# Kernel optimization log

Hardware: AMD Instinct MI355X
Metric: run time of the kernel (lower is better)

Reference implementation:

```python
import jax, jax.numpy as jnp
import numpy as np

TILE = 128
NEG = -1e10


def rotate_half(x):
    half = x.shape[-1] // 2
    return jnp.concatenate([-x[..., half:], x[..., :half]], axis=-1)


def setup_inputs() -> dict:
    key = jax.random.key(0)
    ks = jax.random.split(key, 7)
    B, S, E, H, D, K = 1, 4096, 2048, 16, 128, 8
    T = S // TILE
    x = jax.random.normal(ks[0], (B, S, E), jnp.float32)
    wq = jax.random.normal(ks[1], (E, H * D), jnp.float32) * 0.02
    wk = jax.random.normal(ks[2], (E, H * D), jnp.float32) * 0.02
    wv = jax.random.normal(ks[3], (E, H * D), jnp.float32) * 0.02
    wo = jax.random.normal(ks[4], (H * D, E), jnp.float32) * 0.02
    rope_angles = jax.random.uniform(ks[5], (S, D // 2), jnp.float32)
    anchor_indices = jax.random.randint(ks[6], (B, H, T, K), 0, T).astype(jnp.int32)
    return {"x": x, "wq": wq, "wk": wk, "wv": wv, "wo": wo,
            "rope_angles": rope_angles, "anchor_indices": anchor_indices}


def reference(x, wq, wk, wv, wo, rope_angles, anchor_indices):
    B, S, E = x.shape
    D = rope_angles.shape[1] * 2          # head_dim
    H = wq.shape[1] // D                  # num_heads
    T = S // TILE                         # num_tiles
    sm_scale = 1.0 / jnp.sqrt(jnp.float32(D))

    # QKV projections -> [B, H, S, D]
    def proj(w):
        return (x @ w).reshape(B, S, H, D).transpose(0, 2, 1, 3).astype(jnp.float32)
    q, k, v = proj(wq), proj(wk), proj(wv)

    # RoPE (half-split / rotate_half format)
    cos = jnp.cos(rope_angles)[None, None]   # [1,1,S,D/2]
    sin = jnp.sin(rope_angles)[None, None]
    cos_f = jnp.concatenate([cos, cos], axis=-1)
    sin_f = jnp.concatenate([sin, sin], axis=-1)
    q = q * cos_f + rotate_half(q) * sin_f
    k = k * cos_f + rotate_half(k) * sin_f

    # Tile selection: anchor tiles + local (diagonal) tile -> [B,H,T,K+1]
    local = jnp.broadcast_to(jnp.arange(T, dtype=jnp.int32)[None, None, :, None], (B, H, T, 1))
    tile_sel = jnp.concatenate([anchor_indices, local], axis=-1)
    L = tile_sel.shape[-1] * TILE            # sparse_len
    token_idx = tile_sel[..., None] * TILE + jnp.arange(TILE, dtype=jnp.int32)[None, None, None, None, :]
    flat_idx = jnp.clip(token_idx.reshape(B, H, T, L), 0, S - 1)  # [B,H,T,L]

    # Gather selected KV tiles: [B,H,T,L,D]
    def gather(kv):
        return jnp.take_along_axis(kv, flat_idx.reshape(B, H, T * L, 1), axis=2).reshape(B, H, T, L, D)
    k_sp, v_sp = gather(k), gather(v)

    # Block-sparse attention per query tile
    q_t = q.reshape(B, H, T, TILE, D)
    logits = jnp.einsum('bhtqd,bhtkd->bhtqk', q_t, k_sp) * sm_scale
    q_pos = jnp.arange(S).reshape(T, TILE)
    future = flat_idx[:, :, :, None, :] > q_pos[None, None, :, :, None]  # causal mask on gathered keys
    logits = jnp.where(future, NEG, logits)
    w = jax.nn.softmax(logits, axis=-1)
    all_masked = jnp.all(future, axis=-1, keepdims=True)
    w = jnp.where(all_masked, 0.0, w)
    w = jnp.where(jnp.isnan(w), 0.0, w)
    out = jnp.einsum('bhtqk,bhtkd->bhtqd', w, v_sp)

    out = out.reshape(B, H, S, D).transpose(0, 2, 1, 3).reshape(B, S, H * D)
    return out @ wo
```

## Files before the change

kernel.cpp:

```cpp
#include <hip/hip_runtime.h>
#include <stdint.h>

typedef unsigned short u16;
typedef unsigned int u32;

#define S_LEN 4096
#define EMB 2048
#define NH 16
#define HD 128
#define HDTOT 2048
#define T_TILES 32
#define KANCH 8
#define SM_SCALE 0.088388347648318447f

typedef __bf16 bf16x8 __attribute__((ext_vector_type(8)));
typedef float f32x4 __attribute__((ext_vector_type(4)));

typedef const __attribute__((address_space(1))) u32 ga_u32;
typedef __attribute__((address_space(3))) u32 lds_u32;

__device__ __forceinline__ u16 f2bf(float f) {
  u32 b = __builtin_bit_cast(u32, f);
  b = (b + 0x7FFFu + ((b >> 16) & 1u)) >> 16;
  return (u16)b;
}
__device__ __forceinline__ float bf2f(u16 u) {
  return __builtin_bit_cast(float, ((u32)u) << 16);
}
__device__ __forceinline__ f32x4 mfma16(bf16x8 a, bf16x8 b, f32x4 c) {
  return __builtin_amdgcn_mfma_f32_16x16x32_bf16(a, b, c, 0, 0, 0);
}

#define ASM_LGKM0 do { asm volatile("s_waitcnt lgkmcnt(0)" ::: "memory"); \
                       __builtin_amdgcn_sched_barrier(0); } while (0)
#define ASM_VMC(n) do { asm volatile("s_waitcnt vmcnt(" #n ")" ::: "memory"); \
                        __builtin_amdgcn_sched_barrier(0); } while (0)

__global__ __launch_bounds__(256) void k_prep(
    const float* __restrict__ x, u16* __restrict__ xb,
    const float* __restrict__ w0, const float* __restrict__ w1,
    const float* __restrict__ w2, const float* __restrict__ w3,
    u16* __restrict__ o0, u16* __restrict__ o1,
    u16* __restrict__ o2, u16* __restrict__ o3,
    const float* __restrict__ ang, float2* __restrict__ tab) {
  __shared__ float tile[64][68];
  const int bid = blockIdx.x;
  const int tid = threadIdx.x;
  if (bid < 8192) {
    int i = (bid * 256 + tid) * 4;
    float4 v = *(const float4*)(x + i);
    ushort4 o;
    o.x = f2bf(v.x); o.y = f2bf(v.y); o.z = f2bf(v.z); o.w = f2bf(v.w);
    *(ushort4*)(xb + i) = o;
  } else if (bid < 12288) {
    int idx = bid - 8192;
    int z = idx >> 10, rem = idx & 1023;
    int n0 = (rem & 31) * 64, k0 = (rem >> 5) * 64;
    const float* w; u16* o;
    if (z == 0)      { w = w0; o = o0; }
    else if (z == 1) { w = w1; o = o1; }
    else if (z == 2) { w = w2; o = o2; }
    else             { w = w3; o = o3; }
    int r = tid >> 4, cq = (tid & 15) << 2;
    for (int p = 0; p < 4; ++p) {
      float4 v = *(const float4*)(w + (size_t)(k0 + r + p * 16) * EMB + n0 + cq);
      tile[r + p * 16][cq + 0] = v.x;
      tile[r + p * 16][cq + 1] = v.y;
      tile[r + p * 16][cq + 2] = v.z;
      tile[r + p * 16][cq + 3] = v.w;
    }
    __syncthreads();
    for (int p = 0; p < 4; ++p) {
      int rn = r + p * 16;
      ushort4 u;
      u.x = f2bf(tile[cq + 0][rn]);
      u.y = f2bf(tile[cq + 1][rn]);
      u.z = f2bf(tile[cq + 2][rn]);
      u.w = f2bf(tile[cq + 3][rn]);
      *(ushort4*)(o + (size_t)(n0 + rn) * EMB + k0 + cq) = u;
    }
  } else {
    int i = (bid - 12288) * 256 + tid;
    float a = ang[i];
    float s, c;
    __sincosf(a, &s, &c);
    tab[i] = make_float2(c, s);
  }
}

__global__ __launch_bounds__(256) void k_transpose_v(const u16* __restrict__ v,
                                                     u16* __restrict__ vt) {
  __shared__ u16 tile[64][72];
  int n0 = blockIdx.x * 64, s0 = blockIdx.y * 64;
  int tid = threadIdx.x;
  int r = tid >> 4, cq = (tid & 15) << 2;
  for (int p = 0; p < 4; ++p) {
    ushort4 u = *(const ushort4*)(v + (size_t)(s0 + r + p * 16) * HDTOT + n0 + cq);
    tile[r + p * 16][cq + 0] = u.x;
    tile[r + p * 16][cq + 1] = u.y;
    tile[r + p * 16][cq + 2] = u.z;
    tile[r + p * 16][cq + 3] = u.w;
  }
  __syncthreads();
  for (int p = 0; p < 4; ++p) {
    int rn = r + p * 16;
    ushort4 o;
    o.x = tile[cq + 0][rn];
    o.y = tile[cq + 1][rn];
    o.z = tile[cq + 2][rn];
    o.w = tile[cq + 3][rn];
    *(ushort4*)(vt + (size_t)(n0 + rn) * S_LEN + s0 + cq) = o;
  }
}

template <bool BF16OUT>
__device__ __forceinline__ void gemm_body(const u16* __restrict__ A,
                                          const u16* __restrict__ Bt,
                                          void* __restrict__ Cv,
                                          int N, int K, int m0, int n0,
                                          u16* As, u16* Bs) {
  const int tid = threadIdx.x;
  const int lane = tid & 63, wave = tid >> 6;
  const int quad = lane >> 4, l16 = lane & 15;
  const int wm = (wave >> 1) * 64, wn = (wave & 1) * 64;
  const int sw = (quad ^ (l16 & 3) ^ ((l16 >> 2) & 3)) * 8;
  f32x4 acc[4][4] = {};

  const int flat0 = wave * 1024 + lane * 16;
  for (int kt = 0; kt < K; kt += 32) {
    for (int half = 0; half < 2; ++half) {
      int flat = flat0 + half * 4096;
      int row = flat >> 6;
      int gl = (flat >> 4) & 3;
      int colb = ((gl ^ (row & 3) ^ ((row >> 2) & 3)) << 4);
      const char* ga = (const char*)A + ((size_t)(m0 + row) * K + kt) * 2 + colb;
      const char* gb = (const char*)Bt + ((size_t)(n0 + row) * K + kt) * 2 + colb;
      int loff = wave * 1024 + half * 4096;
      __builtin_amdgcn_global_load_lds((ga_u32*)ga, (lds_u32*)((char*)As + loff), 16, 0, 0);
      __builtin_amdgcn_global_load_lds((ga_u32*)gb, (lds_u32*)((char*)Bs + loff), 16, 0, 0);
    }
    __syncthreads();
    bf16x8 af[4], bfr[4];
    for (int mt = 0; mt < 4; ++mt)
      af[mt] = *(const bf16x8*)(As + (wm + mt * 16 + l16) * 32 + sw);
    for (int nt = 0; nt < 4; ++nt)
      bfr[nt] = *(const bf16x8*)(Bs + (wn + nt * 16 + l16) * 32 + sw);
    for (int mt = 0; mt < 4; ++mt)
      for (int nt = 0; nt < 4; ++nt)
        acc[mt][nt] = mfma16(af[mt], bfr[nt], acc[mt][nt]);
    __syncthreads();
  }
  for (int mt = 0; mt < 4; ++mt) {
    int row = m0 + wm + mt * 16 + quad * 4;
    for (int nt = 0; nt < 4; ++nt) {
      int col = n0 + wn + nt * 16 + l16;
      for (int r = 0; r < 4; ++r) {
        if (BF16OUT)
          ((u16*)Cv)[(size_t)(row + r) * N + col] = f2bf(acc[mt][nt][r]);
        else
          ((float*)Cv)[(size_t)(row + r) * N + col] = acc[mt][nt][r];
      }
    }
  }
}

template <bool BF16OUT>
__global__ __launch_bounds__(256) void k_gemm(const u16* __restrict__ A,
                                              const u16* __restrict__ Bt,
                                              void* __restrict__ Cv,
                                              int N, int K) {
  __shared__ __align__(16) u16 As[128 * 32];
  __shared__ __align__(16) u16 Bs[128 * 32];
  gemm_body<BF16OUT>(A, Bt, Cv, N, K, blockIdx.y * 128, blockIdx.x * 128, As, Bs);
}

__global__ __launch_bounds__(512, 2) void k_gemm256_qkv(
    const u16* __restrict__ A, const u16* __restrict__ Bt,
    u16* __restrict__ q, u16* __restrict__ k, u16* __restrict__ v,
    const float2* __restrict__ cssn) {
  __shared__ __align__(16) u16 lds[65536];
  int flat = blockIdx.y * 24 + blockIdx.x;
  flat = (flat & 7) * 48 + (flat >> 3);
  const int bx = flat % 24, by = flat / 24;
  const int m0 = by * 256;
  const int n0g = bx * 256;
  u16* out = (bx < 8) ? q : ((bx < 16) ? k : v);
  const int ncol0 = (bx & 7) * 256;

  const int tid = threadIdx.x;
  const int lane = tid & 63, wave = tid >> 6;
  const int quad = lane >> 4, l16 = lane & 15;
  const int wm = wave >> 2, wn = wave & 3;
  const int sw0 = (quad ^ (l16 & 7)) * 8, sw1 = ((quad ^ (l16 & 7)) ^ 4) * 8;

  size_t soff[2];
#pragma unroll
  for (int p = 0; p < 2; ++p) {
    int fl = p * 8192 + tid * 16;
    int row = fl >> 7;
    int gsw = ((fl >> 4) & 7) ^ (row & 7);
    soff[p] = (size_t)row * 4096 + (size_t)(gsw * 16);
  }
  const char* aBase = (const char*)A + (size_t)m0 * 4096;
  const char* bBase = (const char*)Bt + (size_t)n0g * 4096;
  const int dstW = wave * 1024;

  auto stA = [&](int buf, int half, int kt) {
#pragma unroll
    for (int p = 0; p < 2; ++p)
      __builtin_amdgcn_global_load_lds(
          (ga_u32*)(aBase + (size_t)half * 524288 + (size_t)kt * 128 + soff[p]),
          (lds_u32*)((char*)lds + buf * 32768 + half * 16384 + p * 8192 + dstW),
          16, 0, 0);
  };
  auto stB = [&](int buf, int half, int kt) {
#pragma unroll
    for (int p = 0; p < 2; ++p)
      __builtin_amdgcn_global_load_lds(
          (ga_u32*)(bBase + (size_t)half * 524288 + (size_t)kt * 128 + soff[p]),
          (lds_u32*)((char*)lds + 65536 + buf * 32768 + half * 16384 + p * 8192 + dstW),
          16, 0, 0);
  };
  const u16* aRd = lds + wm * 8192 + l16 * 64;
  const u16* bRd = lds + 32768 + (wn * 16 + l16) * 64;

  f32x4 acc[8][4] = {};

  stB(0, 0, 0); stA(0, 0, 0); stB(0, 1, 0); stA(0, 1, 0);
  stB(1, 0, 1); stA(1, 0, 1);
  ASM_VMC(4);
  __builtin_amdgcn_s_barrier();

  const int NT = EMB / 64;
  for (int j = 0; j < NT; ++j) {
    const int par = j & 1;
    const u16* aT = aRd + par * 16384;
    const u16* bT = bRd + par * 16384;
    bf16x8 af[4][2], blo[2][2], bhi[2][2];
#pragma unroll
    for (int m = 0; m < 4; ++m) {
      af[m][0] = *(const bf16x8*)(aT + m * 1024 + sw0);
      af[m][1] = *(const bf16x8*)(aT + m * 1024 + sw1);
    }
#pragma unroll
    for (int n = 0; n < 2; ++n) {
      blo[n][0] = *(const bf16x8*)(bT + n * 4096 + sw0);
      blo[n][1] = *(const bf16x8*)(bT + n * 4096 + sw1);
    }
    if (j + 1 < NT) stB(1 - par, 1, j + 1);
    __builtin_amdgcn_s_barrier();
    ASM_LGKM0;
    __builtin_amdgcn_s_setprio(1);
#pragma unroll
    for (int m = 0; m < 4; ++m)
#pragma unroll
      for (int n = 0; n < 2; ++n) {
        acc[m][n] = mfma16(af[m][0], blo[n][0], acc[m][n]);
        acc[m][n] = mfma16(af[m][1], blo[n][1], acc[m][n]);
      }
    __builtin_amdgcn_s_setprio(0);
    __builtin_amdgcn_s_barrier();
#pragma unroll
    for (int n = 0; n < 2; ++n) {
      bhi[n][0] = *(const bf16x8*)(bT + (n + 2) * 4096 + sw0);
      bhi[n][1] = *(const bf16x8*)(bT + (n + 2) * 4096 + sw1);
    }
    if (j + 1 < NT) stA(1 - par, 1, j + 1);
    __builtin_amdgcn_s_barrier();
    ASM_LGKM0;
    __builtin_amdgcn_s_setprio(1);
#pragma unroll
    for (int m = 0; m < 4; ++m)
#pragma unroll
      for (int n = 0; n < 2; ++n) {
        acc[m][n + 2] = mfma16(af[m][0], bhi[n][0], acc[m][n + 2]);
        acc[m][n + 2] = mfma16(af[m][1], bhi[n][1], acc[m][n + 2]);
      }
    __builtin_amdgcn_s_setprio(0);
    __builtin_amdgcn_s_barrier();
#pragma unroll
    for (int m = 0; m < 4; ++m) {
      af[m][0] = *(const bf16x8*)(aT + (m + 4) * 1024 + sw0);
      af[m][1] = *(const bf16x8*)(aT + (m + 4) * 1024 + sw1);
    }
    if (j + 2 < NT) stB(par, 0, j + 2);
    __builtin_amdgcn_s_barrier();
    ASM_LGKM0;
    __builtin_amdgcn_s_setprio(1);
#pragma unroll
    for (int m = 0; m < 4; ++m)
#pragma unroll
      for (int n = 0; n < 2; ++n) {
        acc[m + 4][n + 2] = mfma16(af[m][0], bhi[n][0], acc[m + 4][n + 2]);
        acc[m + 4][n + 2] = mfma16(af[m][1], bhi[n][1], acc[m + 4][n + 2]);
      }
    __builtin_amdgcn_s_setprio(0);
    __builtin_amdgcn_s_barrier();
    if (j + 2 < NT) stA(par, 0, j + 2);
    __builtin_amdgcn_s_barrier();
    __builtin_amdgcn_s_setprio(1);
#pragma unroll
    for (int m = 0; m < 4; ++m)
#pragma unroll
      for (int n = 0; n < 2; ++n) {
        acc[m + 4][n] = mfma16(af[m][0], blo[n][0], acc[m + 4][n]);
        acc[m + 4][n] = mfma16(af[m][1], blo[n][1], acc[m + 4][n]);
      }
    __builtin_amdgcn_s_setprio(0);
    if (j == NT - 2) { ASM_VMC(0); } else { ASM_VMC(4); }
    __builtin_amdgcn_s_barrier();
  }

  if (bx < 16) {
    const int dcol = wn * 16 + l16;
#pragma unroll
    for (int m = 0; m < 8; ++m) {
      int srow = m0 + wm * 128 + m * 16 + quad * 4;
#pragma unroll
      for (int r = 0; r < 4; ++r) {
        int s = srow + r;
        float2 cs2 = cssn[s * 64 + dcol];
        u16* op = out + (size_t)s * HDTOT + ncol0 + dcol;
        float lo0 = acc[m][0][r], hi0 = acc[m][1][r];
        op[0]   = f2bf(lo0 * cs2.x - hi0 * cs2.y);
        op[64]  = f2bf(hi0 * cs2.x + lo0 * cs2.y);
        float lo1 = acc[m][2][r], hi1 = acc[m][3][r];
        op[128] = f2bf(lo1 * cs2.x - hi1 * cs2.y);
        op[192] = f2bf(hi1 * cs2.x + lo1 * cs2.y);
      }
    }
  } else {
#pragma unroll
    for (int m = 0; m < 8; ++m) {
      int row = m0 + wm * 128 + m * 16 + quad * 4;
#pragma unroll
      for (int n = 0; n < 4; ++n) {
        int col = ncol0 + (wn + 4 * n) * 16 + l16;
#pragma unroll
        for (int r = 0; r < 4; ++r)
          out[(size_t)(row + r) * HDTOT + col] = f2bf(acc[m][n][r]);
      }
    }
  }
}

__device__ __forceinline__ bf16x8 ldsfrag(const u16* __restrict__ sbuf, int r, int cb) {
  return *(const bf16x8*)(sbuf + r * 128 + (((cb ^ (r & 15)) << 3)));
}
__device__ __forceinline__ bf16x8 ldsfragV(const u16* __restrict__ sbuf, int r, int cb) {
  return *(const bf16x8*)(sbuf + r * 64 + (((cb ^ (r & 7)) << 3)));
}

__global__ __launch_bounds__(256, 2) void k_attn(const u16* __restrict__ q,
                                                 const u16* __restrict__ k,
                                                 const u16* __restrict__ vt,
                                                 const int* __restrict__ anch,
                                                 u16* __restrict__ out) {
  __shared__ __align__(16) u16 bufK[2][64 * 128];
  __shared__ __align__(16) u16 bufV[2][128 * 64];
  __shared__ int s_tj[KANCH + 1];
  __shared__ int s_nv;
  const int i = blockIdx.x;
  const int p2 = (i ^ (i >> 8)) & 1;
  const int c = i >> 1;
  const int t = p2 ? (15 - (c >> 4)) : (16 + (c >> 4));
  const int h = c & 15;
  const int tid = threadIdx.x;
  const int lane = tid & 63, wave = tid >> 6;
  const int quad = lane >> 4, l16 = lane & 15;
  const int wq0 = wave * 32;

  int offK[4], offV[4];
#pragma unroll
  for (int p = 0; p < 4; ++p) {
    int krow = (wave * 4 + p) * 4 + (lane >> 4);
    int kcol = ((lane & 15) ^ (krow & 15)) << 3;
    offK[p] = (krow * HDTOT + kcol) * 2;
    int vrow = (wave * 4 + p) * 8 + (lane >> 3);
    int vcol = ((lane & 7) ^ (vrow & 7)) << 3;
    offV[p] = (vrow * S_LEN + vcol) * 2;
  }

  if (tid == 0) {
    int nv = 0;
    for (int j = 0; j < KANCH; ++j) {
      int tj = anch[((h * T_TILES) + t) * KANCH + j];
      if (tj <= t) s_tj[nv++] = tj;
    }
    s_tj[nv++] = t;
    s_nv = nv;
  }

  {
    const char* gq = (const char*)(q + (size_t)(t * 128) * HDTOT + h * HD);
    char* lq = (char*)bufK + wave * 8192;
#pragma unroll
    for (int p = 0; p < 8; ++p) {
      int qrow = (wave * 8 + p) * 4 + (lane >> 4);
      int qcol = ((lane & 15) ^ (qrow & 15)) << 3;
      __builtin_amdgcn_global_load_lds((ga_u32*)(gq + (qrow * HDTOT + qcol) * 2),
                                       (lds_u32*)(lq + p * 1024), 16, 0, 0);
    }
  }
  __syncthreads();

  bf16x8 qf[2][4];
#pragma unroll
  for (int qh = 0; qh < 2; ++qh)
#pragma unroll
    for (int ks = 0; ks < 4; ++ks)
      qf[qh][ks] = ldsfrag(&bufK[0][0], wq0 + qh * 16 + l16, ks * 4 + quad);

  const int nv2 = 2 * s_nv;
  const char* kh = (const char*)(k + h * HD);
  const char* vh = (const char*)(vt + (size_t)(h * HD) * S_LEN);

  __syncthreads();

  {
    int key0 = s_tj[0] * 128;
    const char* gk = kh + (size_t)key0 * (HDTOT * 2);
    const char* gv = vh + (size_t)key0 * 2;
    char* lk = (char*)bufK[0] + wave * 4096;
    char* lv = (char*)bufV[0] + wave * 4096;
#pragma unroll
    for (int p = 0; p < 4; ++p) {
      __builtin_amdgcn_global_load_lds((ga_u32*)(gk + offK[p]),
                                       (lds_u32*)(lk + p * 1024), 16, 0, 0);
      __builtin_amdgcn_global_load_lds((ga_u32*)(gv + offV[p]),
                                       (lds_u32*)(lv + p * 1024), 16, 0, 0);
    }
  }

  f32x4 oacc[2][8] = {};
  float m_st[2] = {-1e30f, -1e30f};
  float l_st[2] = {0.f, 0.f};

  for (int it = 0; it < nv2; ++it) {
    const int par = it & 1;
    const u16* K_c = bufK[par];
    const u16* V_c = bufV[par];
    const int tj = s_tj[it >> 1];
    const int half = it & 1;
    const bool diag = (tj == t);

    __syncthreads();

    if (it + 1 < nv2) {
      int inx = it + 1;
      int key0 = s_tj[inx >> 1] * 128 + (inx & 1) * 64;
      const char* gk = kh + (size_t)key0 * (HDTOT * 2);
      const char* gv = vh + (size_t)key0 * 2;
      char* lk = (char*)bufK[1 - par] + wave * 4096;
      char* lv = (char*)bufV[1 - par] + wave * 4096;
#pragma unroll
      for (int p = 0; p < 4; ++p) {
        __builtin_amdgcn_global_load_lds((ga_u32*)(gk + offK[p]),
                                         (lds_u32*)(lk + p * 1024), 16, 0, 0);
        __builtin_amdgcn_global_load_lds((ga_u32*)(gv + offV[p]),
                                         (lds_u32*)(lv + p * 1024), 16, 0, 0);
      }
    }

    f32x4 sacc[2][4] = {};
    __builtin_amdgcn_s_setprio(1);
#pragma unroll
    for (int ks = 0; ks < 4; ++ks)
#pragma unroll
      for (int a = 0; a < 4; ++a) {
        bf16x8 kf = ldsfrag(K_c, a * 16 + l16, ks * 4 + quad);
        sacc[0][a] = mfma16(kf, qf[0][ks], sacc[0][a]);
        sacc[1][a] = mfma16(kf, qf[1][ks], sacc[1][a]);
      }
    __builtin_amdgcn_s_setprio(0);

    u32 pl[2][4], ph[2][4];
    float alpha[2];
    bool needR[2];
#pragma unroll
    for (int qh = 0; qh < 2; ++qh) {
      const int qr = wq0 + qh * 16 + l16;
      const int kb = half * 64;
      float amax[4];
#pragma unroll
      for (int a = 0; a < 4; ++a) {
        f32x4 s4 = sacc[qh][a];
#pragma unroll
        for (int r = 0; r < 4; ++r) {
          float sv = s4[r] * SM_SCALE;
          if (diag && (kb + a * 16 + quad * 4 + r > qr)) sv = -1e30f;
          s4[r] = sv;
        }
        sacc[qh][a] = s4;
        amax[a] = fmaxf(fmaxf(s4[0], s4[1]), fmaxf(s4[2], s4[3]));
      }
      float rmax = fmaxf(fmaxf(amax[0], amax[1]), fmaxf(amax[2], amax[3]));
      rmax = fmaxf(rmax, __shfl_xor(rmax, 16));
      rmax = fmaxf(rmax, __shfl_xor(rmax, 32));
      bool skip = __all(rmax <= m_st[qh]);
      float mnew = skip ? m_st[qh] : fmaxf(m_st[qh], rmax);
      alpha[qh] = skip ? 1.0f : __expf(m_st[qh] - mnew);
      needR[qh] = !skip;
      m_st[qh] = mnew;
      float rs0 = 0.f, rs1 = 0.f;
#pragma unroll
      for (int a = 0; a < 4; ++a) {
        f32x4 s4 = sacc[qh][a];
        float e0 = __expf(s4[0] - mnew);
        float e1 = __expf(s4[1] - mnew);
        float e2 = __expf(s4[2] - mnew);
        float e3 = __expf(s4[3] - mnew);
        rs0 += (e0 + e1);
        rs1 += (e2 + e3);
        pl[qh][a] = __builtin_amdgcn_perm(__builtin_bit_cast(u32, e1) + 0x8000u,
                                          __builtin_bit_cast(u32, e0) + 0x8000u,
                                          0x07060302u);
        ph[qh][a] = __builtin_amdgcn_perm(__builtin_bit_cast(u32, e3) + 0x8000u,
                                          __builtin_bit_cast(u32, e2) + 0x8000u,
                                          0x07060302u);
      }
      float rsum = rs0 + rs1;
      rsum += __shfl_xor(rsum, 16);
      rsum += __shfl_xor(rsum, 32);
      l_st[qh] = skip ? (l_st[qh] + rsum) : (l_st[qh] * alpha[qh] + rsum);
    }

#pragma unroll
    for (int qh = 0; qh < 2; ++qh) {
      if (needR[qh]) {
        f32x4 av;
#pragma unroll
        for (int r = 0; r < 4; ++r)
          av[r] = __shfl(alpha[qh], (lane & 48) | (quad * 4 + r));
#pragma unroll
        for (int nt = 0; nt < 8; ++nt) {
          f32x4 o4 = oacc[qh][nt];
          o4[0] *= av[0]; o4[1] *= av[1]; o4[2] *= av[2]; o4[3] *= av[3];
          oacc[qh][nt] = o4;
        }
      }
    }

    const int srcA = ((quad & 1) << 5) + l16;
    const int srcB = srcA + 16;
    const int hi = quad >> 1;
#pragma unroll
    for (int cc = 0; cc < 2; ++cc) {
      bf16x8 pa[2];
#pragma unroll
      for (int qh = 0; qh < 2; ++qh) {
        u32 x0 = __shfl(pl[qh][2 * cc], srcA), x1 = __shfl(ph[qh][2 * cc], srcA);
        u32 x2 = __shfl(pl[qh][2 * cc], srcB), x3 = __shfl(ph[qh][2 * cc], srcB);
        u32 y0 = __shfl(pl[qh][2 * cc + 1], srcA), y1 = __shfl(ph[qh][2 * cc + 1], srcA);
        u32 y2 = __shfl(pl[qh][2 * cc + 1], srcB), y3 = __shfl(ph[qh][2 * cc + 1], srcB);
        uint4 w;
        w.x = hi ? y0 : x0;
        w.y = hi ? y1 : x1;
        w.z = hi ? y2 : x2;
        w.w = hi ? y3 : x3;
        pa[qh] = __builtin_bit_cast(bf16x8, w);
      }
      __builtin_amdgcn_s_setprio(1);
#pragma unroll
      for (int nt = 0; nt < 8; ++nt) {
        bf16x8 vf = ldsfragV(V_c, nt * 16 + l16, cc * 4 + quad);
        oacc[0][nt] = mfma16(pa[0], vf, oacc[0][nt]);
        oacc[1][nt] = mfma16(pa[1], vf, oacc[1][nt]);
      }
      __builtin_amdgcn_s_setprio(0);
    }
  }

#pragma unroll
  for (int qh = 0; qh < 2; ++qh) {
    float linv = 1.0f / l_st[qh];
    f32x4 iv;
#pragma unroll
    for (int r = 0; r < 4; ++r)
      iv[r] = __shfl(linv, (lane & 48) | (quad * 4 + r));
#pragma unroll
    for (int r = 0; r < 4; ++r) {
      size_t srow_o = (size_t)(t * 128 + wq0 + qh * 16 + quad * 4 + r);
#pragma unroll
      for (int nt = 0; nt < 8; ++nt)
        out[srow_o * HDTOT + h * HD + nt * 16 + l16] = f2bf(oacc[qh][nt][r] * iv[r]);
    }
  }
}

extern "C" void kernel_launch(void* const* d_in, const int* in_sizes, int n_in,
                              void* d_out, int out_size, void* d_ws, size_t ws_size,
                              hipStream_t stream) {
  const float* x   = (const float*)d_in[0];
  const float* wq  = (const float*)d_in[1];
  const float* wk  = (const float*)d_in[2];
  const float* wv  = (const float*)d_in[3];
  const float* wo  = (const float*)d_in[4];
  const float* ang = (const float*)d_in[5];
  const int* anch  = (const int*)d_in[6];

  char* ws = (char*)d_ws;
  const size_t SZ_SE = (size_t)S_LEN * HDTOT * sizeof(u16);
  const size_t SZ_W  = (size_t)EMB * EMB * sizeof(u16);
  u16* xb   = (u16*)(ws);
  u16* qb   = (u16*)(ws + SZ_SE);
  u16* kb   = (u16*)(ws + 2 * SZ_SE);
  u16* vb   = (u16*)(ws + 3 * SZ_SE);
  u16* vtb  = (u16*)(ws + 4 * SZ_SE);
  u16* attn = (u16*)(ws + 5 * SZ_SE);
  u16* wqT  = (u16*)(ws + 6 * SZ_SE);
  u16* wkT  = (u16*)(ws + 6 * SZ_SE + SZ_W);
  u16* wvT  = (u16*)(ws + 6 * SZ_SE + 2 * SZ_W);
  u16* woT  = (u16*)(ws + 6 * SZ_SE + 3 * SZ_W);

  float2* cssn = (float2*)d_out;

  k_prep<<<13312, 256, 0, stream>>>(x, xb, wq, wk, wv, wo, wqT, wkT, wvT, woT,
                                    ang, cssn);
  k_gemm256_qkv<<<dim3(24, 16), 512, 0, stream>>>(xb, wqT, qb, kb, vb, cssn);
  k_transpose_v<<<dim3(32, 64), 256, 0, stream>>>(vb, vtb);
  k_attn<<<dim3(512), 256, 0, stream>>>(qb, kb, vtb, anch, attn);
  k_gemm<false><<<dim3(16, 32), 256, 0, stream>>>(attn, woT, d_out, EMB, HDTOT);
}
```

Before: 384.4 us.

## Shrink QKV GEMM tile to 128x256 for more blocks and smaller LDS

The fused QKV projection GEMM moves from 256x256 tiles to 128x256 tiles. This doubles the grid to 768 blocks, shrinks LDS to 96KB, and restructures the k-loop into three MFMA phases with matching async loads. The CU swizzle and the RoPE epilogue are adjusted to match. The intent is better wave balance across the 256 CUs than 384 large tiles give. The cost is lower arithmetic intensity per block, since each block reloads more B data relative to its output.

```diff
diff --git a/kernel.cpp b/kernel.cpp
--- a/kernel.cpp
+++ b/kernel.cpp
@@ -174,15 +174,15 @@
   gemm_body<BF16OUT>(A, Bt, Cv, N, K, blockIdx.y * 128, blockIdx.x * 128, As, Bs);
 }
 
-__global__ __launch_bounds__(512, 2) void k_gemm256_qkv(
+__global__ __launch_bounds__(512, 1) void k_gemm_qkv(
     const u16* __restrict__ A, const u16* __restrict__ Bt,
     u16* __restrict__ q, u16* __restrict__ k, u16* __restrict__ v,
     const float2* __restrict__ cssn) {
-  __shared__ __align__(16) u16 lds[65536];
-  int flat = blockIdx.y * 24 + blockIdx.x;
-  flat = (flat & 7) * 48 + (flat >> 3);
+  __shared__ __align__(16) u16 lds[49152];
+  int orig = blockIdx.y * 24 + blockIdx.x;
+  int flat = (orig & 7) * 96 + (orig >> 3);
   const int bx = flat % 24, by = flat / 24;
-  const int m0 = by * 256;
+  const int m0 = by * 128;
   const int n0g = bx * 256;
   u16* out = (bx < 8) ? q : ((bx < 16) ? k : v);
   const int ncol0 = (bx & 7) * 256;
@@ -193,129 +193,124 @@
   const int wm = wave >> 2, wn = wave & 3;
   const int sw0 = (quad ^ (l16 & 7)) * 8, sw1 = ((quad ^ (l16 & 7)) ^ 4) * 8;
 
-  size_t soff[2];
-#pragma unroll
-  for (int p = 0; p < 2; ++p) {
+  u32 soff[4];
+#pragma unroll
+  for (int p = 0; p < 4; ++p) {
     int fl = p * 8192 + tid * 16;
     int row = fl >> 7;
     int gsw = ((fl >> 4) & 7) ^ (row & 7);
-    soff[p] = (size_t)row * 4096 + (size_t)(gsw * 16);
+    soff[p] = (u32)row * 4096 + (u32)(gsw * 16);
   }
   const char* aBase = (const char*)A + (size_t)m0 * 4096;
   const char* bBase = (const char*)Bt + (size_t)n0g * 4096;
   const int dstW = wave * 1024;
 
-  auto stA = [&](int buf, int half, int kt) {
+  auto stA = [&](int buf, int kt) {
 #pragma unroll
     for (int p = 0; p < 2; ++p)
       __builtin_amdgcn_global_load_lds(
-          (ga_u32*)(aBase + (size_t)half * 524288 + (size_t)kt * 128 + soff[p]),
-          (lds_u32*)((char*)lds + buf * 32768 + half * 16384 + p * 8192 + dstW),
-          16, 0, 0);
+          (ga_u32*)(aBase + (size_t)kt * 128 + soff[p]),
+          (lds_u32*)((char*)lds + buf * 16384 + p * 8192 + dstW), 16, 0, 0);
   };
-  auto stB = [&](int buf, int half, int kt) {
+  auto stB0 = [&](int buf, int kt) {
 #pragma unroll
     for (int p = 0; p < 2; ++p)
       __builtin_amdgcn_global_load_lds(
-          (ga_u32*)(bBase + (size_t)half * 524288 + (size_t)kt * 128 + soff[p]),
-          (lds_u32*)((char*)lds + 65536 + buf * 32768 + half * 16384 + p * 8192 + dstW),
-          16, 0, 0);
+          (ga_u32*)(bBase + (size_t)kt * 128 + soff[p]),
+          (lds_u32*)((char*)lds + 32768 + buf * 32768 + p * 8192 + dstW), 16, 0, 0);
   };
-  const u16* aRd = lds + wm * 8192 + l16 * 64;
-  const u16* bRd = lds + 32768 + (wn * 16 + l16) * 64;
-
-  f32x4 acc[8][4] = {};
-
-  stB(0, 0, 0); stA(0, 0, 0); stB(0, 1, 0); stA(0, 1, 0);
-  stB(1, 0, 1); stA(1, 0, 1);
-  ASM_VMC(4);
+  auto stB1 = [&](int buf, int kt) {
+#pragma unroll
+    for (int p = 2; p < 4; ++p)
+      __builtin_amdgcn_global_load_lds(
+          (ga_u32*)(bBase + (size_t)kt * 128 + soff[p]),
+          (lds_u32*)((char*)lds + 32768 + buf * 32768 + p * 8192 + dstW), 16, 0, 0);
+  };
+
+  const u16* aRd = lds + (wm * 64 + l16) * 64;
+  const u16* bRd = lds + 16384 + (wn * 16 + l16) * 64;
+
+  f32x4 acc[4][4] = {};
+
+  stB0(0, 0); stB1(0, 0); stA(0, 0);
+  stB0(1, 1);
+  ASM_VMC(2);
   __builtin_amdgcn_s_barrier();
 
   const int NT = EMB / 64;
   for (int j = 0; j < NT; ++j) {
     const int par = j & 1;
-    const u16* aT = aRd + par * 16384;
+    const u16* aT = aRd + par * 8192;
     const u16* bT = bRd + par * 16384;
-    bf16x8 af[4][2], blo[2][2], bhi[2][2];
-#pragma unroll
-    for (int m = 0; m < 4; ++m) {
+    bf16x8 af[4][2], bfr[4][2];
+#pragma unroll
+    for (int m = 0; m < 2; ++m) {
       af[m][0] = *(const bf16x8*)(aT + m * 1024 + sw0);
       af[m][1] = *(const bf16x8*)(aT + m * 1024 + sw1);
     }
 #pragma unroll
     for (int n = 0; n < 2; ++n) {
-      blo[n][0] = *(const bf16x8*)(bT + n * 4096 + sw0);
-      blo[n][1] = *(const bf16x8*)(bT + n * 4096 + sw1);
-    }
-    if (j + 1 < NT) stB(1 - par, 1, j + 1);
+      bfr[n][0] = *(const bf16x8*)(bT + n * 4096 + sw0);
+      bfr[n][1] = *(const bf16x8*)(bT + n * 4096 + sw1);
+    }
+    if (j + 1 < NT) stB1(1 - par, j + 1);
     __builtin_amdgcn_s_barrier();
     ASM_LGKM0;
     __builtin_amdgcn_s_setprio(1);
 #pragma unroll
-    for (int m = 0; m < 4; ++m)
+    for (int m = 0; m < 2; ++m)
 #pragma unroll
       for (int n = 0; n < 2; ++n) {
-        acc[m][n] = mfma16(af[m][0], blo[n][0], acc[m][n]);
-        acc[m][n] = mfma16(af[m][1], blo[n][1], acc[m][n]);
+        acc[m][n] = mfma16(af[m][0], bfr[n][0], acc[m][n]);
+        acc[m][n] = mfma16(af[m][1], bfr[n][1], acc[m][n]);
       }
     __builtin_amdgcn_s_setprio(0);
     __builtin_amdgcn_s_barrier();
 #pragma unroll
-    for (int n = 0; n < 2; ++n) {
-      bhi[n][0] = *(const bf16x8*)(bT + (n + 2) * 4096 + sw0);
-      bhi[n][1] = *(const bf16x8*)(bT + (n + 2) * 4096 + sw1);
-    }
-    if (j + 1 < NT) stA(1 - par, 1, j + 1);
+    for (int n = 2; n < 4; ++n) {
+      bfr[n][0] = *(const bf16x8*)(bT + n * 4096 + sw0);
+      bfr[n][1] = *(const bf16x8*)(bT + n * 4096 + sw1);
+    }
+    if (j + 1 < NT) stA(1 - par, j + 1);
     __builtin_amdgcn_s_barrier();
     ASM_LGKM0;
     __builtin_amdgcn_s_setprio(1);
 #pragma unroll
-    for (int m = 0; m < 4; ++m)
-#pragma unroll
-      for (int n = 0; n < 2; ++n) {
-        acc[m][n + 2] = mfma16(af[m][0], bhi[n][0], acc[m][n + 2]);
-        acc[m][n + 2] = mfma16(af[m][1], bhi[n][1], acc[m][n + 2]);
+    for (int m = 0; m < 2; ++m)
+#pragma unroll
+      for (int n = 2; n < 4; ++n) {
+        acc[m][n] = mfma16(af[m][0], bfr[n][0], acc[m][n]);
+        acc[m][n] = mfma16(af[m][1], bfr[n][1], acc[m][n]);
       }
     __builtin_amdgcn_s_setprio(0);
     __builtin_amdgcn_s_barrier();
 #pragma unroll
-    for (int m = 0; m < 4; ++m) {
-      af[m][0] = *(const bf16x8*)(aT + (m + 4) * 1024 + sw0);
-      af[m][1] = *(const bf16x8*)(aT + (m + 4) * 1024 + sw1);
-    }
-    if (j + 2 < NT) stB(par, 0, j + 2);
+    for (int m = 2; m < 4; ++m) {
+      af[m][0] = *(const bf16x8*)(aT + m * 1024 + sw0);
+      af[m][1] = *(const bf16x8*)(aT + m * 1024 + sw1);
+    }
+    if (j + 2 < NT) stB0(par, j + 2);
     __builtin_amdgcn_s_barrier();
     ASM_LGKM0;
     __builtin_amdgcn_s_setprio(1);
 #pragma unroll
-    for (int m = 0; m < 4; ++m)
-#pragma unroll
-      for (int n = 0; n < 2; ++n) {
-        acc[m + 4][n + 2] = mfma16(af[m][0], bhi[n][0], acc[m + 4][n + 2]);
-        acc[m + 4][n + 2] = mfma16(af[m][1], bhi[n][1], acc[m + 4][n + 2]);
+    for (int m = 2; m < 4; ++m)
+#pragma unroll
+      for (int n = 0; n < 4; ++n) {
+        acc[m][n] = mfma16(af[m][0], bfr[n][0], acc[m][n]);
+        acc[m][n] = mfma16(af[m][1], bfr[n][1], acc[m][n]);
       }
     __builtin_amdgcn_s_setprio(0);
-    __builtin_amdgcn_s_barrier();
-    if (j + 2 < NT) stA(par, 0, j + 2);
-    __builtin_amdgcn_s_barrier();
-    __builtin_amdgcn_s_setprio(1);
-#pragma unroll
-    for (int m = 0; m < 4; ++m)
-#pragma unroll
-      for (int n = 0; n < 2; ++n) {
-        acc[m + 4][n] = mfma16(af[m][0], blo[n][0], acc[m + 4][n]);
-        acc[m + 4][n] = mfma16(af[m][1], blo[n][1], acc[m + 4][n]);
-      }
-    __builtin_amdgcn_s_setprio(0);
-    if (j == NT - 2) { ASM_VMC(0); } else { ASM_VMC(4); }
-    __builtin_amdgcn_s_barrier();
+    if (j < NT - 2) { ASM_VMC(2); }
+    else if (j == NT - 2) { ASM_VMC(0); }
+    if (j < NT - 1) __builtin_amdgcn_s_barrier();
   }
 
   if (bx < 16) {
     const int dcol = wn * 16 + l16;
 #pragma unroll
-    for (int m = 0; m < 8; ++m) {
-      int srow = m0 + wm * 128 + m * 16 + quad * 4;
+    for (int m = 0; m < 4; ++m) {
+      int srow = m0 + wm * 64 + m * 16 + quad * 4;
 #pragma unroll
       for (int r = 0; r < 4; ++r) {
         int s = srow + r;
@@ -331,8 +326,8 @@
     }
   } else {
 #pragma unroll
-    for (int m = 0; m < 8; ++m) {
-      int row = m0 + wm * 128 + m * 16 + quad * 4;
+    for (int m = 0; m < 4; ++m) {
+      int row = m0 + wm * 64 + m * 16 + quad * 4;
 #pragma unroll
       for (int n = 0; n < 4; ++n) {
         int col = ncol0 + (wn + 4 * n) * 16 + l16;
@@ -617,7 +612,7 @@
 
   k_prep<<<13312, 256, 0, stream>>>(x, xb, wq, wk, wv, wo, wqT, wkT, wvT, woT,
                                     ang, cssn);
-  k_gemm256_qkv<<<dim3(24, 16), 512, 0, stream>>>(xb, wqT, qb, kb, vb, cssn);
+  k_gemm_qkv<<<dim3(24, 32), 512, 0, stream>>>(xb, wqT, qb, kb, vb, cssn);
   k_transpose_v<<<dim3(32, 64), 256, 0, stream>>>(vb, vtb);
   k_attn<<<dim3(512), 256, 0, stream>>>(qb, kb, vtb, anch, attn);
   k_gemm<false><<<dim3(16, 32), 256, 0, stream>>>(attn, woT, d_out, EMB, HDTOT);
```

New measurement: 374.7 us. 1.03x faster.
